# Performance work log

Measured on AMD Instinct MI355X. Metric: run time of the kernel, lower is better.

The kernel has to match this reference:

```python
import jax, jax.numpy as jnp
import numpy as np

K_NN = 16  # number of nearest neighbors (module init arg k)


def setup_inputs() -> dict:
    key = jax.random.key(0)
    k1, k2 = jax.random.split(key)
    xyz = jax.random.normal(k1, (8, 16384, 3), dtype=jnp.float32)
    centers = jax.random.normal(k2, (8, 1024, 3), dtype=jnp.float32)
    return {"xyz": xyz, "centers": centers}


def reference(xyz, centers):
    # avoiding the (B, N, K, 3) broadcast intermediate of the original while
    # computing the same torch.norm(xyz - centers, dim=-1) math.
    x_sq = jnp.sum(xyz * xyz, axis=-1)          # (B, N)
    c_sq = jnp.sum(centers * centers, axis=-1)  # (B, K)
    cross = jnp.einsum('bnd,bkd->bnk', xyz, centers)  # (B, N, K)
    d2 = x_sq[:, :, None] + c_sq[None if False else slice(None), None, :] - 2.0 * cross
    dist = jnp.sqrt(jnp.maximum(d2, 0.0))       # (B, N, K)
    # torch.topk(dist, k, dim=1, largest=False, sorted=True):
    # smallest-k over the N (points) axis, per center.
    neg = -jnp.transpose(dist, (0, 2, 1))       # (B, K, N)
    _, idx = jax.lax.top_k(neg, K_NN)           # (B, K, k), ascending distance
    return jnp.transpose(idx, (0, 2, 1))        # (B, k, K) to match torch dim=1 topk
```

## Files before the change

### kernel.cpp

```cpp
#include <hip/hip_runtime.h>
#include <stdint.h>

#define BB    8
#define NN    16384
#define KK    1024
#define KNN   16
#define QTR   (NN / 4)
#define QGRP  (QTR / 4)
#define NG16  (NN / 16)
#define GCAP  48
#define SCAP  192

typedef unsigned long long u64;
typedef float f32x2 __attribute__((ext_vector_type(2)));

__device__ __forceinline__ f32x2 pk_fma(f32x2 a, f32x2 b, f32x2 c) {
    f32x2 d;
    asm("v_pk_fma_f32 %0, %1, %2, %3" : "=v"(d) : "v"(a), "v"(b), "v"(c));
    return d;
}
__device__ __forceinline__ f32x2 pk_mul(f32x2 a, f32x2 b) {
    f32x2 d;
    asm("v_pk_mul_f32 %0, %1, %2" : "=v"(d) : "v"(a), "v"(b));
    return d;
}
__device__ __forceinline__ f32x2 pk_add(f32x2 a, f32x2 b) {
    f32x2 d;
    asm("v_pk_add_f32 %0, %1, %2" : "=v"(d) : "v"(a), "v"(b));
    return d;
}

__device__ __forceinline__ u64 shfl_xor_u64(u64 v, int mask) {
    int lo = (int)(uint32_t)v;
    int hi = (int)(uint32_t)(v >> 32);
    lo = __shfl_xor(lo, mask, 64);
    hi = __shfl_xor(hi, mask, 64);
    return ((u64)(uint32_t)hi << 32) | (u64)(uint32_t)lo;
}

__device__ __forceinline__ u64 shfl_u64(u64 v, int src) {
    int lo = __shfl((int)(uint32_t)v, src, 64);
    int hi = __shfl((int)(uint32_t)(v >> 32), src, 64);
    return ((u64)(uint32_t)hi << 32) | (u64)(uint32_t)lo;
}

__device__ __forceinline__ u64 wave_min_u64(u64 v) {
#pragma unroll
    for (int off = 32; off > 0; off >>= 1) {
        u64 o = shfl_xor_u64(v, off);
        v = o < v ? o : v;
    }
    return v;
}

__device__ __forceinline__ void sort64_kv(u64& key, uint32_t& pay, int lane) {
#pragma unroll
    for (int k = 2; k <= 64; k <<= 1) {
#pragma unroll
        for (int j = k >> 1; j > 0; j >>= 1) {
            u64 okey = shfl_xor_u64(key, j);
            uint32_t opay = (uint32_t)__shfl_xor((int)pay, j, 64);
            bool tmin = ((lane & j) == 0) == ((lane & k) == 0);
            bool osm = okey < key;
            bool take = tmin ? osm : !osm;
            if (take) { key = okey; pay = opay; }
        }
    }
}

__device__ __forceinline__ void sort64_k(u64& key, int lane) {
#pragma unroll
    for (int k = 2; k <= 64; k <<= 1) {
#pragma unroll
        for (int j = k >> 1; j > 0; j >>= 1) {
            u64 okey = shfl_xor_u64(key, j);
            bool tmin = ((lane & j) == 0) == ((lane & k) == 0);
            bool osm = okey < key;
            bool take = tmin ? osm : !osm;
            if (take) key = okey;
        }
    }
}

__device__ __forceinline__ float point_d2(const float* xb, int i,
                                          float c0, float c1, float c2, float csq) {
#pragma clang fp contract(off)
    float x0 = xb[i * 3 + 0];
    float x1 = xb[i * 3 + 1];
    float x2 = xb[i * 3 + 2];
    float xsq = (x0 * x0 + x1 * x1) + x2 * x2;
    float cross = __fmaf_rn(x2, c2, __fmaf_rn(x1, c1, x0 * c0));
    float d2 = (xsq + csq) - 2.0f * cross;
    return d2 < 0.0f ? 0.0f : d2;
}

__device__ __attribute__((noinline)) int fallback_scan(const float* xb,
                                                       float c0, float c1, float c2,
                                                       float csq, int lane) {
    u64 list[KNN];
#pragma unroll
    for (int j = 0; j < KNN; ++j) list[j] = ~0ull;
    for (int i = lane; i < NN; i += 64) {
        float d2 = point_d2(xb, i, c0, c1, c2, csq);
        float dist = __fsqrt_rn(d2);
        u64 key = ((u64)__float_as_uint(dist) << 32) | (u64)(uint32_t)i;
        if (key < list[KNN - 1]) {
#pragma unroll
            for (int j = 0; j < KNN; ++j) {
                bool lt = key < list[j];
                u64 lo = lt ? key : list[j];
                u64 hi = lt ? list[j] : key;
                list[j] = lo;
                key = hi;
            }
        }
    }
    int res = 0;
    for (int it = 0; it < KNN; ++it) {
        u64 best = wave_min_u64(list[0]);
        if (it == lane) res = (int)(uint32_t)best;
        if (list[0] == best) {
#pragma unroll
            for (int j = 0; j < KNN - 1; ++j) list[j] = list[j + 1];
            list[KNN - 1] = ~0ull;
        }
    }
    return res;
}

__device__ __forceinline__ float sixteenth_smallest(float m, int lane) {
    uint32_t u = __float_as_uint(m);
    uint32_t s = (u & 0x80000000u) ? ~u : (u | 0x80000000u);
    u64 v = ((u64)s << 32) | (unsigned)lane;
#pragma unroll
    for (int k = 2; k <= 64; k <<= 1) {
#pragma unroll
        for (int j = k >> 1; j > 0; j >>= 1) {
            u64 o = shfl_xor_u64(v, j);
            bool up = (lane & k) == 0;
            bool takeMin = ((lane & j) == 0) == up;
            u64 mn = v < o ? v : o;
            u64 mx = v < o ? o : v;
            v = takeMin ? mn : mx;
        }
    }
    uint32_t sb = (uint32_t)__shfl((int)(uint32_t)(v >> 32), 15, 64);
    uint32_t ub = (sb & 0x80000000u) ? (sb ^ 0x80000000u) : ~sb;
    return __uint_as_float(ub);
}

__device__ __forceinline__ void load_pairs_aos(const float4* x4, int g,
                                               f32x2& xl, f32x2& xh,
                                               f32x2& yl, f32x2& yh,
                                               f32x2& zl, f32x2& zh,
                                               f32x2& sl, f32x2& sh) {
    float4 f0 = x4[g * 3 + 0];
    float4 f1 = x4[g * 3 + 1];
    float4 f2 = x4[g * 3 + 2];
    xl = f32x2{f0.x, f0.w};  yl = f32x2{f0.y, f1.x};  zl = f32x2{f0.z, f1.y};
    xh = f32x2{f1.z, f2.y};  yh = f32x2{f1.w, f2.z};  zh = f32x2{f2.x, f2.w};
    sl = pk_add(pk_add(pk_mul(xl, xl), pk_mul(yl, yl)), pk_mul(zl, zl));
    sh = pk_add(pk_add(pk_mul(xh, xh), pk_mul(yh, yh)), pk_mul(zh, zh));
}

__global__ __launch_bounds__(256, 8) void knn_kernel(const float* __restrict__ xyz,
                                                     const float* __restrict__ centers,
                                                     int* __restrict__ out) {
#pragma clang fp contract(off)
    const int q = (int)(threadIdx.x >> 6);
    const int lane = (int)(threadIdx.x & 63);
    const int cbase = (int)blockIdx.x * 4;
    const int b = cbase >> 10;

    __shared__ float    s_gmin[4][NG16];
    __shared__ uint32_t s_glist[4][GCAP];
    __shared__ uint32_t s_idx[4][SCAP];
    __shared__ int      s_gcnt[4];
    __shared__ int      s_cnt[4];

    f32x2 nx[4], ny[4], nz[4];
#pragma unroll
    for (int c = 0; c < 4; ++c) {
        float a0 = -2.0f * centers[(cbase + c) * 3 + 0];
        float a1 = -2.0f * centers[(cbase + c) * 3 + 1];
        float a2 = -2.0f * centers[(cbase + c) * 3 + 2];
        nx[c] = f32x2{a0, a0};
        ny[c] = f32x2{a1, a1};
        nz[c] = f32x2{a2, a2};
    }

    const float* xb = xyz + (size_t)b * NN * 3;
    const float4* x4 = (const float4*)xb;
    const int gbase = q * QGRP;

    if (threadIdx.x < 4) { s_gcnt[threadIdx.x] = 0; s_cnt[threadIdx.x] = 0; }

#pragma unroll 2
    for (int s = 0; s < QGRP / 64; ++s) {
        int g = gbase + s * 64 + lane;
        f32x2 xl, xh, yl, yh, zl, zh, sl, sh;
        load_pairs_aos(x4, g, xl, xh, yl, yh, zl, zh, sl, sh);
        float gm[4];
#pragma unroll
        for (int c = 0; c < 4; ++c) {
            f32x2 dl = pk_fma(xl, nx[c], pk_fma(yl, ny[c], pk_fma(zl, nz[c], sl)));
            f32x2 dh = pk_fma(xh, nx[c], pk_fma(yh, ny[c], pk_fma(zh, nz[c], sh)));
            float v = fminf(fminf(dl.x, dl.y), fminf(dh.x, dh.y));
            v = fminf(v, __shfl_xor(v, 1, 64));
            v = fminf(v, __shfl_xor(v, 2, 64));
            gm[c] = v;
        }
        if ((lane & 3) == 0) {
            int gi = g >> 2;
#pragma unroll
            for (int c = 0; c < 4; ++c) s_gmin[c][gi] = gm[c];
        }
    }
    __syncthreads();

    float lm = __builtin_inff();
#pragma unroll
    for (int it = 0; it < NG16 / 64; ++it)
        lm = fminf(lm, s_gmin[q][it * 64 + lane]);
    float t = sixteenth_smallest(lm, lane);
    const float Uq = t + fabsf(t) * 1e-5f + 5e-4f;

#pragma unroll
    for (int it = 0; it < NG16 / 64; ++it) {
        int gi = it * 64 + lane;
        if (s_gmin[q][gi] <= Uq) {
            int pos = atomicAdd(&s_gcnt[q], 1);
            if (pos < GCAP) s_glist[q][pos] = (uint32_t)gi;
        }
    }
    __syncthreads();

    const int ng = s_gcnt[q];
    bool ok = (ng <= GCAP);

    if (ok) {
        for (int j = lane; j < ng * 4; j += 64) {
            int lg = (int)s_glist[q][j >> 2] * 4 + (j & 3);
            f32x2 xl, xh, yl, yh, zl, zh, sl, sh;
            load_pairs_aos(x4, lg, xl, xh, yl, yh, zl, zh, sl, sh);
            f32x2 dl = pk_fma(xl, nx[q], pk_fma(yl, ny[q], pk_fma(zl, nz[q], sl)));
            f32x2 dh = pk_fma(xh, nx[q], pk_fma(yh, ny[q], pk_fma(zh, nz[q], sh)));
            int ibase = lg * 4;
            if (dl.x <= Uq) {
                int pos = atomicAdd(&s_cnt[q], 1);
                if (pos < SCAP) s_idx[q][pos] = (uint32_t)(ibase + 0);
            }
            if (dl.y <= Uq) {
                int pos = atomicAdd(&s_cnt[q], 1);
                if (pos < SCAP) s_idx[q][pos] = (uint32_t)(ibase + 1);
            }
            if (dh.x <= Uq) {
                int pos = atomicAdd(&s_cnt[q], 1);
                if (pos < SCAP) s_idx[q][pos] = (uint32_t)(ibase + 2);
            }
            if (dh.y <= Uq) {
                int pos = atomicAdd(&s_cnt[q], 1);
                if (pos < SCAP) s_idx[q][pos] = (uint32_t)(ibase + 3);
            }
        }
    }

    const int cc = cbase + q;
    const float c0 = centers[cc * 3 + 0];
    const float c1 = centers[cc * 3 + 1];
    const float c2 = centers[cc * 3 + 2];
    const float csq = (c0 * c0 + c1 * c1) + c2 * c2;
    const int total = s_cnt[q];
    ok = ok && (total <= SCAP);

    uint32_t res;
    if (ok) {
        u64 l0 = ~0ull, l1 = ~0ull, l2 = ~0ull, l3 = ~0ull;
        for (int j = lane; j < total; j += 64) {
            int idx = (int)s_idx[q][j];
            float d2 = point_d2(xb, idx, c0, c1, c2, csq);
            u64 key = ((u64)__float_as_uint(__fsqrt_rn(d2)) << 32) | (u64)(uint32_t)idx;
            bool tt;
            tt = key < l0; { u64 lo = tt ? key : l0, hi = tt ? l0 : key; l0 = lo; key = hi; }
            tt = key < l1; { u64 lo = tt ? key : l1, hi = tt ? l1 : key; l1 = lo; key = hi; }
            tt = key < l2; { u64 lo = tt ? key : l2, hi = tt ? l2 : key; l2 = lo; key = hi; }
            tt = key < l3; { u64 lo = tt ? key : l3, hi = tt ? l3 : key; l3 = lo; key = hi; }
        }
        u64 key = l0;
        uint32_t pay = (uint32_t)lane;
        sort64_kv(key, pay, lane);
        int pos = lane >> 2, elem = lane & 3;
        int sid = __shfl((int)pay, pos, 64);
        u64 g0 = shfl_u64(l0, sid);
        u64 g1 = shfl_u64(l1, sid);
        u64 g2 = shfl_u64(l2, sid);
        u64 g3 = shfl_u64(l3, sid);
        u64 gk = (elem == 0) ? g0 : (elem == 1) ? g1 : (elem == 2) ? g2 : g3;
        sort64_k(gk, lane);
        res = (uint32_t)gk;
    } else {
        res = (uint32_t)fallback_scan(xb, c0, c1, c2, csq, lane);
    }

    if (lane < KNN) {
        out[((size_t)b * KNN + lane) * KK + (cc & 1023)] = (int)res;
    }
}

extern "C" void kernel_launch(void* const* d_in, const int* in_sizes, int n_in,
                              void* d_out, int out_size, void* d_ws, size_t ws_size,
                              hipStream_t stream) {
    const float* xyz = (const float*)d_in[0];
    const float* centers = (const float*)d_in[1];
    int* out = (int*)d_out;
    (void)d_ws; (void)ws_size;

    const int nblocks = BB * KK / 4;
    hipLaunchKernelGGL(knn_kernel, dim3(nblocks), dim3(256), 0, stream,
                       xyz, centers, out);
}
```

Baseline: 95.79 us.

## Compute per-group minima in registers, use min3, and add a single-sort fast path

```diff
diff --git a/kernel.cpp b/kernel.cpp
--- a/kernel.cpp
+++ b/kernel.cpp
@@ -27,6 +27,11 @@
 __device__ __forceinline__ f32x2 pk_add(f32x2 a, f32x2 b) {
     f32x2 d;
     asm("v_pk_add_f32 %0, %1, %2" : "=v"(d) : "v"(a), "v"(b));
+    return d;
+}
+__device__ __forceinline__ float min3f(float a, float b, float c) {
+    float d;
+    asm("v_min3_f32 %0, %1, %2, %3" : "=v"(d) : "v"(a), "v"(b), "v"(c));
     return d;
 }
 
@@ -195,35 +200,35 @@
 
     if (threadIdx.x < 4) { s_gcnt[threadIdx.x] = 0; s_cnt[threadIdx.x] = 0; }
 
-#pragma unroll 2
-    for (int s = 0; s < QGRP / 64; ++s) {
-        int g = gbase + s * 64 + lane;
-        f32x2 xl, xh, yl, yh, zl, zh, sl, sh;
-        load_pairs_aos(x4, g, xl, xh, yl, yh, zl, zh, sl, sh);
-        float gm[4];
-#pragma unroll
-        for (int c = 0; c < 4; ++c) {
-            f32x2 dl = pk_fma(xl, nx[c], pk_fma(yl, ny[c], pk_fma(zl, nz[c], sl)));
-            f32x2 dh = pk_fma(xh, nx[c], pk_fma(yh, ny[c], pk_fma(zh, nz[c], sh)));
-            float v = fminf(fminf(dl.x, dl.y), fminf(dh.x, dh.y));
-            v = fminf(v, __shfl_xor(v, 1, 64));
-            v = fminf(v, __shfl_xor(v, 2, 64));
-            gm[c] = v;
-        }
-        if ((lane & 3) == 0) {
-            int gi = g >> 2;
-#pragma unroll
-            for (int c = 0; c < 4; ++c) s_gmin[c][gi] = gm[c];
-        }
+    for (int t = 0; t < 4; ++t) {
+        const int lg0 = gbase + t * 256 + lane * 4;
+        float acc[4];
+#pragma unroll
+        for (int c = 0; c < 4; ++c) acc[c] = __builtin_inff();
+#pragma unroll
+        for (int u = 0; u < 4; ++u) {
+            f32x2 xl, xh, yl, yh, zl, zh, sl, sh;
+            load_pairs_aos(x4, lg0 + u, xl, xh, yl, yh, zl, zh, sl, sh);
+#pragma unroll
+            for (int c = 0; c < 4; ++c) {
+                f32x2 dl = pk_fma(xl, nx[c], pk_fma(yl, ny[c], pk_fma(zl, nz[c], sl)));
+                f32x2 dh = pk_fma(xh, nx[c], pk_fma(yh, ny[c], pk_fma(zh, nz[c], sh)));
+                acc[c] = min3f(acc[c], dl.x, dl.y);
+                acc[c] = min3f(acc[c], dh.x, dh.y);
+            }
+        }
+        const int gi = lg0 >> 2;
+#pragma unroll
+        for (int c = 0; c < 4; ++c) s_gmin[c][gi] = acc[c];
     }
     __syncthreads();
 
     float lm = __builtin_inff();
 #pragma unroll
-    for (int it = 0; it < NG16 / 64; ++it)
-        lm = fminf(lm, s_gmin[q][it * 64 + lane]);
-    float t = sixteenth_smallest(lm, lane);
-    const float Uq = t + fabsf(t) * 1e-5f + 5e-4f;
+    for (int it = 0; it < NG16 / 128; ++it)
+        lm = min3f(lm, s_gmin[q][it * 128 + lane], s_gmin[q][it * 128 + 64 + lane]);
+    float t16 = sixteenth_smallest(lm, lane);
+    const float Uq = t16 + fabsf(t16) * 1e-5f + 5e-4f;
 
 #pragma unroll
     for (int it = 0; it < NG16 / 64; ++it) {
@@ -286,18 +291,23 @@
             tt = key < l2; { u64 lo = tt ? key : l2, hi = tt ? l2 : key; l2 = lo; key = hi; }
             tt = key < l3; { u64 lo = tt ? key : l3, hi = tt ? l3 : key; l3 = lo; key = hi; }
         }
-        u64 key = l0;
-        uint32_t pay = (uint32_t)lane;
-        sort64_kv(key, pay, lane);
-        int pos = lane >> 2, elem = lane & 3;
-        int sid = __shfl((int)pay, pos, 64);
-        u64 g0 = shfl_u64(l0, sid);
-        u64 g1 = shfl_u64(l1, sid);
-        u64 g2 = shfl_u64(l2, sid);
-        u64 g3 = shfl_u64(l3, sid);
-        u64 gk = (elem == 0) ? g0 : (elem == 1) ? g1 : (elem == 2) ? g2 : g3;
-        sort64_k(gk, lane);
-        res = (uint32_t)gk;
+        if (total <= 64) {
+            sort64_k(l0, lane);
+            res = (uint32_t)l0;
+        } else {
+            u64 key = l0;
+            uint32_t pay = (uint32_t)lane;
+            sort64_kv(key, pay, lane);
+            int pos = lane >> 2, elem = lane & 3;
+            int sid = __shfl((int)pay, pos, 64);
+            u64 g0 = shfl_u64(l0, sid);
+            u64 g1 = shfl_u64(l1, sid);
+            u64 g2 = shfl_u64(l2, sid);
+            u64 g3 = shfl_u64(l3, sid);
+            u64 gk = (elem == 0) ? g0 : (elem == 1) ? g1 : (elem == 2) ? g2 : g3;
+            sort64_k(gk, lane);
+            res = (uint32_t)gk;
+        }
     } else {
         res = (uint32_t)fallback_scan(xb, c0, c1, c2, csq, lane);
     }
```

Measured after the change: 107.6 us. 12.3% more time.
